# Optimization experiments

Hardware: AMD Instinct MI355X
Metric: run time of the kernel (lower is better)

Reference implementation:

```python
import jax, jax.numpy as jnp
import numpy as np

N_SRC = 100000
N_DST = 50000
N_EDGES = 1600000
D_IN = 128
D_OUT = 64


def setup_inputs() -> dict:
    key = jax.random.key(0)
    ks = jax.random.split(key, 6)
    x = jax.random.normal(ks[0], (N_SRC, D_IN), dtype=jnp.float32)
    W_l = jax.random.normal(ks[1], (D_IN, D_OUT), dtype=jnp.float32) * (1.0 / np.sqrt(D_IN))
    b_l = jax.random.normal(ks[2], (D_OUT,), dtype=jnp.float32) * 0.01
    W_r = jax.random.normal(ks[3], (D_IN, D_OUT), dtype=jnp.float32) * (1.0 / np.sqrt(D_IN))
    src = jax.random.randint(ks[4], (N_EDGES,), 0, N_SRC, dtype=jnp.int64)
    dst = jax.random.randint(ks[5], (N_EDGES,), 0, N_DST, dtype=jnp.int64)
    edge_index = jnp.stack([src, dst], axis=0)
    return {"x": x, "W_l": W_l, "b_l": b_l, "W_r": W_r,
            "edge_index": edge_index, "n_dst": N_DST}


def reference(x, W_l, b_l, W_r, edge_index, n_dst):
    src, dst = edge_index[0], edge_index[1]
    # gather source features along edges: [E, D_in]
    msgs = x[src]
    # mean aggregation at destination nodes
    agg = jax.ops.segment_sum(msgs, dst, num_segments=n_dst)          # [n_dst, D_in]
    cnt = jax.ops.segment_sum(jnp.ones_like(dst, dtype=x.dtype), dst,
                              num_segments=n_dst)                     # [n_dst]
    mean = agg / jnp.maximum(cnt, 1.0)[:, None]
    x_target = x[:n_dst]
    # SAGEConv: lin_l(mean_agg) + lin_r(x_target)
    out = mean @ W_l + b_l + x_target @ W_r                           # [n_dst, D_out]
    return jax.nn.log_softmax(out, axis=-1)
```

## Files before the change

### kernel.cpp

```cpp
#include <hip/hip_runtime.h>
#include <math.h>

#define DIN  128
#define DOUT 64
#define SLOT 96

__device__ inline unsigned short f2bf(float f) {
    unsigned u = __float_as_uint(f);
    u += 0x7fffu + ((u >> 16) & 1u);
    return (unsigned short)(u >> 16);
}
__device__ inline float bflo(unsigned u) { return __uint_as_float(u << 16); }
__device__ inline float bfhi(unsigned u) { return __uint_as_float(u & 0xffff0000u); }

__global__ void __launch_bounds__(256) build_k(
    const int* __restrict__ ei, unsigned* __restrict__ cnt,
    int* __restrict__ slots,
    const float* __restrict__ x, const float* __restrict__ Wl,
    const float* __restrict__ bl, const float* __restrict__ Wr,
    unsigned short* __restrict__ y, float* __restrict__ zout,
    int E, int nFill, int P, int nyb, int n_src, int n_dst, int cstr)
{
    __shared__ float s_x[16][DIN];
    const int b = blockIdx.x;
    const int fq = b / P;
    const bool isFill = ((b % P) == 0) && (fq < nFill);

    if (isFill) {
        int t = fq * 256 + threadIdx.x;
        int base = t * 8;
        if (base >= E) return;
        if (base + 8 <= E) {
            int4 sa = *(const int4*)(ei + base);
            int4 sb4 = *(const int4*)(ei + base + 4);
            int4 da = *(const int4*)(ei + E + base);
            int4 db = *(const int4*)(ei + E + base + 4);
            unsigned p0 = atomicAdd(&cnt[(size_t)da.x * cstr], 1u);
            unsigned p1 = atomicAdd(&cnt[(size_t)da.y * cstr], 1u);
            unsigned p2 = atomicAdd(&cnt[(size_t)da.z * cstr], 1u);
            unsigned p3 = atomicAdd(&cnt[(size_t)da.w * cstr], 1u);
            unsigned p4 = atomicAdd(&cnt[(size_t)db.x * cstr], 1u);
            unsigned p5 = atomicAdd(&cnt[(size_t)db.y * cstr], 1u);
            unsigned p6 = atomicAdd(&cnt[(size_t)db.z * cstr], 1u);
            unsigned p7 = atomicAdd(&cnt[(size_t)db.w * cstr], 1u);
            if (p0 < SLOT) slots[(size_t)da.x * SLOT + p0] = sa.x;
            if (p1 < SLOT) slots[(size_t)da.y * SLOT + p1] = sa.y;
            if (p2 < SLOT) slots[(size_t)da.z * SLOT + p2] = sa.z;
            if (p3 < SLOT) slots[(size_t)da.w * SLOT + p3] = sa.w;
            if (p4 < SLOT) slots[(size_t)db.x * SLOT + p4] = sb4.x;
            if (p5 < SLOT) slots[(size_t)db.y * SLOT + p5] = sb4.y;
            if (p6 < SLOT) slots[(size_t)db.z * SLOT + p6] = sb4.z;
            if (p7 < SLOT) slots[(size_t)db.w * SLOT + p7] = sb4.w;
        } else {
            for (int i = base; i < E && i < base + 8; ++i) {
                int s = ei[i], d = ei[E + i];
                unsigned p = atomicAdd(&cnt[(size_t)d * cstr], 1u);
                if (p < SLOT) slots[(size_t)d * SLOT + p] = s;
            }
        }
        return;
    }

    const int fillsBefore = (fq + 1 < nFill) ? (fq + 1) : nFill;
    const int pb   = b - fillsBefore;
    const int wave = threadIdx.x >> 6, lane = threadIdx.x & 63;
    const int sb = wave * 4;
    const bool isY = (pb < nyb);
    const int rowBase = (isY ? pb : pb - nyb) * 16 + sb;
    const int nRows = isY ? n_src : n_dst;
    const float* W = isY ? Wl : Wr;

    for (int r = 0; r < 4; ++r) {
        int row = rowBase + r;
        if (row >= nRows) continue;
        float2 v = *(const float2*)(x + (size_t)row * DIN + lane * 2);
        s_x[sb + r][lane * 2]     = v.x;
        s_x[sb + r][lane * 2 + 1] = v.y;
    }
    __syncthreads();

    float a0 = 0.f, a1 = 0.f, a2 = 0.f, a3 = 0.f;
    #pragma unroll 4
    for (int k = 0; k < DIN; ++k) {
        float w = W[k * DOUT + lane];
        a0 += s_x[sb + 0][k] * w;
        a1 += s_x[sb + 1][k] * w;
        a2 += s_x[sb + 2][k] * w;
        a3 += s_x[sb + 3][k] * w;
    }
    float acc[4] = {a0, a1, a2, a3};
    if (isY) {
        for (int r = 0; r < 4; ++r) {
            int row = rowBase + r;
            if (row < nRows) y[(size_t)row * DOUT + lane] = f2bf(acc[r]);
        }
    } else {
        const float bias = bl[lane];
        for (int r = 0; r < 4; ++r) {
            int row = rowBase + r;
            if (row < nRows) zout[(size_t)row * DOUT + lane] = acc[r] + bias;
        }
    }
}

__global__ void __launch_bounds__(256) gather_k(
    const unsigned short* __restrict__ y,
    const unsigned* __restrict__ cnt, const int* __restrict__ slots,
    float* __restrict__ out, int n_dst, int cstr)
{
    const int wave = threadIdx.x >> 6, lane = threadIdx.x & 63;
    const int row = blockIdx.x * 4 + wave;
    if (row >= n_dst) return;

    int deg = (int)cnt[(size_t)row * cstr];
    if (deg > SLOT) deg = SLOT;
    const int g = lane >> 4;
    const int qi = (lane & 15) * 2;
    const int q  = (lane & 15) * 4;
    const unsigned* yw = (const unsigned*)y;

    float4 ac0 = make_float4(0.f,0.f,0.f,0.f);
    float4 ac1 = make_float4(0.f,0.f,0.f,0.f);
    float4 ac2 = make_float4(0.f,0.f,0.f,0.f);
    float4 ac3 = make_float4(0.f,0.f,0.f,0.f);
    const int* srow = slots + (size_t)row * SLOT;

    for (int co = 0; co < deg; co += 64) {
        int rem = deg - co; if (rem > 64) rem = 64;
        int idx = (lane < rem) ? srow[co + lane] : 0;
        for (int i = 0; i < rem; i += 16) {
            int e0 = i + g, e1 = i + 4 + g, e2 = i + 8 + g, e3 = i + 12 + g;
            int s0 = __shfl(idx, e0), s1 = __shfl(idx, e1);
            int s2 = __shfl(idx, e2), s3 = __shfl(idx, e3);
            if (e0 < rem) { uint2 u = *(const uint2*)(yw + (size_t)s0 * 32 + qi);
                ac0.x += bflo(u.x); ac0.y += bfhi(u.x);
                ac0.z += bflo(u.y); ac0.w += bfhi(u.y); }
            if (e1 < rem) { uint2 u = *(const uint2*)(yw + (size_t)s1 * 32 + qi);
                ac1.x += bflo(u.x); ac1.y += bfhi(u.x);
                ac1.z += bflo(u.y); ac1.w += bfhi(u.y); }
            if (e2 < rem) { uint2 u = *(const uint2*)(yw + (size_t)s2 * 32 + qi);
                ac2.x += bflo(u.x); ac2.y += bfhi(u.x);
                ac2.z += bflo(u.y); ac2.w += bfhi(u.y); }
            if (e3 < rem) { uint2 u = *(const uint2*)(yw + (size_t)s3 * 32 + qi);
                ac3.x += bflo(u.x); ac3.y += bfhi(u.x);
                ac3.z += bflo(u.y); ac3.w += bfhi(u.y); }
        }
    }
    float4 acc;
    acc.x = (ac0.x + ac1.x) + (ac2.x + ac3.x);
    acc.y = (ac0.y + ac1.y) + (ac2.y + ac3.y);
    acc.z = (ac0.z + ac1.z) + (ac2.z + ac3.z);
    acc.w = (ac0.w + ac1.w) + (ac2.w + ac3.w);

    acc.x += __shfl_xor(acc.x, 32); acc.y += __shfl_xor(acc.y, 32);
    acc.z += __shfl_xor(acc.z, 32); acc.w += __shfl_xor(acc.w, 32);
    acc.x += __shfl_xor(acc.x, 16); acc.y += __shfl_xor(acc.y, 16);
    acc.z += __shfl_xor(acc.z, 16); acc.w += __shfl_xor(acc.w, 16);

    const float scale = 1.0f / (float)(deg > 0 ? deg : 1);
    const float4 zv = *(const float4*)(out + (size_t)row * DOUT + q);
    float4 v;
    v.x = acc.x * scale + zv.x;
    v.y = acc.y * scale + zv.y;
    v.z = acc.z * scale + zv.z;
    v.w = acc.w * scale + zv.w;

    float m = fmaxf(fmaxf(v.x, v.y), fmaxf(v.z, v.w));
    for (int o = 8; o >= 1; o >>= 1) m = fmaxf(m, __shfl_xor(m, o));
    float s = expf(v.x - m) + expf(v.y - m) + expf(v.z - m) + expf(v.w - m);
    for (int o = 8; o >= 1; o >>= 1) s += __shfl_xor(s, o);
    const float lse = m + logf(s);

    if (lane < 16) {
        float4 o4;
        o4.x = v.x - lse; o4.y = v.y - lse; o4.z = v.z - lse; o4.w = v.w - lse;
        *(float4*)(out + (size_t)row * DOUT + q) = o4;
    }
}

extern "C" void kernel_launch(void* const* d_in, const int* in_sizes, int n_in,
                              void* d_out, int out_size, void* d_ws, size_t ws_size,
                              hipStream_t stream)
{
    const float* x  = (const float*)d_in[0];
    const float* Wl = (const float*)d_in[1];
    const float* bl = (const float*)d_in[2];
    const float* Wr = (const float*)d_in[3];
    const int*   ei = (const int*)d_in[4];

    const int E     = in_sizes[4] / 2;
    const int n_src = in_sizes[0] / DIN;
    const int n_dst = out_size / DOUT;

    int cstr = 16;
    size_t need16 = (size_t)n_dst * cstr * 4 + (size_t)n_dst * SLOT * 4
                  + (size_t)n_src * DOUT * 2;
    if (need16 > ws_size) cstr = 1;

    unsigned*       cnt   = (unsigned*)d_ws;
    int*            slots = (int*)(cnt + (size_t)n_dst * cstr);
    unsigned short* yb    = (unsigned short*)(slots + (size_t)n_dst * SLOT);

    hipMemsetAsync(cnt, 0, (size_t)n_dst * cstr * sizeof(unsigned), stream);

    int nFill = (E + 2047) / 2048;
    int nyb = (n_src + 15) / 16;
    int nzb = (n_dst + 15) / 16;
    int nProj = nyb + nzb;
    int total = nFill + nProj;
    int P = (total + nFill - 1) / nFill;

    build_k<<<total, 256, 0, stream>>>(
        ei, cnt, slots, x, Wl, bl, Wr, yb, (float*)d_out,
        E, nFill, P, nyb, n_src, n_dst, cstr);

    int gG = (n_dst + 3) / 4;
    gather_k<<<gG, 256, 0, stream>>>(yb, cnt, slots, (float*)d_out, n_dst, cstr);
}
```

Before: 247.6 us.

## Register-tile projection GEMM with 64-row blocks and 4x4 per-thread outputs

The projection part of build_k now handles 64 rows per block instead of 16. It loads x into padded shared memory with float4 loads, and each thread computes a 4-row by 4-column output tile using float4 weight reads and FMAs. This is meant to raise arithmetic intensity, cutting global weight loads and shared-memory reads per FMA, and to vectorise the stores. In exchange there are fewer projection blocks interleaved with fill blocks, more shared memory per block, and higher register pressure.

```diff
diff --git a/kernel.cpp b/kernel.cpp
--- a/kernel.cpp
+++ b/kernel.cpp
@@ -4,6 +4,8 @@
 #define DIN  128
 #define DOUT 64
 #define SLOT 96
+#define PROWS 64
+#define XPITCH 132
 
 __device__ inline unsigned short f2bf(float f) {
     unsigned u = __float_as_uint(f);
@@ -21,7 +23,7 @@
     unsigned short* __restrict__ y, float* __restrict__ zout,
     int E, int nFill, int P, int nyb, int n_src, int n_dst, int cstr)
 {
-    __shared__ float s_x[16][DIN];
+    __shared__ float s_x[PROWS * XPITCH];
     const int b = blockIdx.x;
     const int fq = b / P;
     const bool isFill = ((b % P) == 0) && (fq < nFill);
@@ -62,43 +64,84 @@
     }
 
     const int fillsBefore = (fq + 1 < nFill) ? (fq + 1) : nFill;
-    const int pb   = b - fillsBefore;
-    const int wave = threadIdx.x >> 6, lane = threadIdx.x & 63;
-    const int sb = wave * 4;
+    const int pb = b - fillsBefore;
+    const int t  = threadIdx.x;
     const bool isY = (pb < nyb);
-    const int rowBase = (isY ? pb : pb - nyb) * 16 + sb;
+    const int rowBase = (isY ? pb : pb - nyb) * PROWS;
     const int nRows = isY ? n_src : n_dst;
-    const float* W = isY ? Wl : Wr;
-
-    for (int r = 0; r < 4; ++r) {
-        int row = rowBase + r;
-        if (row >= nRows) continue;
-        float2 v = *(const float2*)(x + (size_t)row * DIN + lane * 2);
-        s_x[sb + r][lane * 2]     = v.x;
-        s_x[sb + r][lane * 2 + 1] = v.y;
+    const float* __restrict__ W = isY ? Wl : Wr;
+
+    {
+        const float* xsrc = x + (size_t)rowBase * DIN;
+        #pragma unroll
+        for (int j = 0; j < 8; ++j) {
+            int fi  = t + 256 * j;
+            int row = fi >> 5, c4 = fi & 31;
+            if (rowBase + row < nRows) {
+                float4 v = *(const float4*)(xsrc + (size_t)fi * 4);
+                *(float4*)(&s_x[row * XPITCH + c4 * 4]) = v;
+            }
+        }
     }
     __syncthreads();
 
-    float a0 = 0.f, a1 = 0.f, a2 = 0.f, a3 = 0.f;
-    #pragma unroll 4
-    for (int k = 0; k < DIN; ++k) {
-        float w = W[k * DOUT + lane];
-        a0 += s_x[sb + 0][k] * w;
-        a1 += s_x[sb + 1][k] * w;
-        a2 += s_x[sb + 2][k] * w;
-        a3 += s_x[sb + 3][k] * w;
-    }
-    float acc[4] = {a0, a1, a2, a3};
+    const int cg = t & 15;
+    const int rg = t >> 4;
+    const int r0 = rg * 4;
+    const float* wp = W + cg * 4;
+
+    float4 acc0 = {0.f,0.f,0.f,0.f};
+    float4 acc1 = {0.f,0.f,0.f,0.f};
+    float4 acc2 = {0.f,0.f,0.f,0.f};
+    float4 acc3 = {0.f,0.f,0.f,0.f};
+
+#define ROWFMA(acc, xv)                                                                     \
+    acc.x = fmaf(xv.w, w3.x, fmaf(xv.z, w2.x, fmaf(xv.y, w1.x, fmaf(xv.x, w0.x, acc.x)))); \
+    acc.y = fmaf(xv.w, w3.y, fmaf(xv.z, w2.y, fmaf(xv.y, w1.y, fmaf(xv.x, w0.y, acc.y)))); \
+    acc.z = fmaf(xv.w, w3.z, fmaf(xv.z, w2.z, fmaf(xv.y, w1.z, fmaf(xv.x, w0.z, acc.z)))); \
+    acc.w = fmaf(xv.w, w3.w, fmaf(xv.z, w2.w, fmaf(xv.y, w1.w, fmaf(xv.x, w0.w, acc.w))));
+
+    #pragma unroll 2
+    for (int k = 0; k < DIN; k += 4) {
+        float4 w0 = *(const float4*)(wp + (size_t)(k + 0) * DOUT);
+        float4 w1 = *(const float4*)(wp + (size_t)(k + 1) * DOUT);
+        float4 w2 = *(const float4*)(wp + (size_t)(k + 2) * DOUT);
+        float4 w3 = *(const float4*)(wp + (size_t)(k + 3) * DOUT);
+        float4 x0 = *(const float4*)(&s_x[(r0 + 0) * XPITCH + k]);
+        float4 x1 = *(const float4*)(&s_x[(r0 + 1) * XPITCH + k]);
+        float4 x2 = *(const float4*)(&s_x[(r0 + 2) * XPITCH + k]);
+        float4 x3 = *(const float4*)(&s_x[(r0 + 3) * XPITCH + k]);
+        ROWFMA(acc0, x0)
+        ROWFMA(acc1, x1)
+        ROWFMA(acc2, x2)
+        ROWFMA(acc3, x3)
+    }
+#undef ROWFMA
+
     if (isY) {
+        float4 av[4] = {acc0, acc1, acc2, acc3};
+        #pragma unroll
         for (int r = 0; r < 4; ++r) {
-            int row = rowBase + r;
-            if (row < nRows) y[(size_t)row * DOUT + lane] = f2bf(acc[r]);
+            int row = rowBase + r0 + r;
+            if (row < nRows) {
+                uint2 pk;
+                pk.x = (unsigned)f2bf(av[r].x) | ((unsigned)f2bf(av[r].y) << 16);
+                pk.y = (unsigned)f2bf(av[r].z) | ((unsigned)f2bf(av[r].w) << 16);
+                *(uint2*)(y + (size_t)row * DOUT + cg * 4) = pk;
+            }
         }
     } else {
-        const float bias = bl[lane];
+        const float4 bv = *(const float4*)(bl + cg * 4);
+        float4 av[4] = {acc0, acc1, acc2, acc3};
+        #pragma unroll
         for (int r = 0; r < 4; ++r) {
-            int row = rowBase + r;
-            if (row < nRows) zout[(size_t)row * DOUT + lane] = acc[r] + bias;
+            int row = rowBase + r0 + r;
+            if (row < nRows) {
+                float4 o;
+                o.x = av[r].x + bv.x; o.y = av[r].y + bv.y;
+                o.z = av[r].z + bv.z; o.w = av[r].w + bv.w;
+                *(float4*)(zout + (size_t)row * DOUT + cg * 4) = o;
+            }
         }
     }
 }
@@ -204,8 +247,8 @@
     hipMemsetAsync(cnt, 0, (size_t)n_dst * cstr * sizeof(unsigned), stream);
 
     int nFill = (E + 2047) / 2048;
-    int nyb = (n_src + 15) / 16;
-    int nzb = (n_dst + 15) / 16;
+    int nyb = (n_src + PROWS - 1) / PROWS;
+    int nzb = (n_dst + PROWS - 1) / PROWS;
     int nProj = nyb + nzb;
     int total = nFill + nProj;
     int P = (total + nFill - 1) / nFill;
```

New measurement: 233.9 us. 5.5% less time.
